# Optimization experiments

Hardware: AMD Instinct MI355X
Metric: run time of the kernel (lower is better)

## Reference

```python
import jax, jax.numpy as jnp
from jax import lax
import numpy as np

MAX_D = 4  # max_displacement


def conv3x3(x, w, b):
    # x: [B,Cin,H,W], w: [Cout,Cin,3,3], SAME padding (pad=1)
    y = lax.conv_general_dilated(
        x, w, window_strides=(1, 1), padding='SAME',
        dimension_numbers=('NCHW', 'OIHW', 'NCHW'))
    return y + b[None, :, None, None]


def compute_cost_volume(f1, f2, d):
    # roll+mask in the torch code == shift with zero padding:
    # cv[idx,h,w] = mean_c f1[c,h,w] * f2[c,h-i,w-j] (zero outside bounds)
    B, C, H, W = f1.shape
    pad = jnp.pad(f2, ((0, 0), (0, 0), (d, d), (d, d)))
    slices = []
    for i in range(-d, d + 1):
        for j in range(-d, d + 1):
            shifted = lax.dynamic_slice(pad, (0, 0, d - i, d - j), (B, C, H, W))
            slices.append((f1 * shifted).sum(axis=1) / C)  # [B,H,W]
    return jnp.stack(slices, axis=1)  # [B,81,H,W]


def setup_inputs() -> dict:
    key = jax.random.key(0)
    ks = jax.random.split(key, 10)
    B, C, H, W = 16, 64, 128, 128
    cv_ch = (2 * MAX_D + 1) ** 2  # 81
    def w_init(k, shape):
        fan_in = shape[1] * shape[2] * shape[3]
        return jax.random.normal(k, shape, dtype=jnp.float32) * np.float32(np.sqrt(2.0 / fan_in))
    return {
        'f1': jax.random.normal(ks[0], (B, C, H, W), dtype=jnp.float32),
        'f2_warped': jax.random.normal(ks[1], (B, C, H, W), dtype=jnp.float32),
        'w1': w_init(ks[2], (128, C + cv_ch, 3, 3)),
        'b1': jnp.zeros((128,), dtype=jnp.float32),
        'w2': w_init(ks[3], (64, 128, 3, 3)),
        'b2': jnp.zeros((64,), dtype=jnp.float32),
        'w3': w_init(ks[4], (32, 64, 3, 3)),
        'b3': jnp.zeros((32,), dtype=jnp.float32),
        'w4': w_init(ks[5], (2, 32, 3, 3)),
        'b4': jnp.zeros((2,), dtype=jnp.float32),
    }


def reference(f1, f2_warped, w1, b1, w2, b2, w3, b3, w4, b4):
    cv = compute_cost_volume(f1, f2_warped, MAX_D)       # [B,81,H,W]
    x = jnp.concatenate([f1, cv], axis=1)                # [B,145,H,W]
    x = jax.nn.relu(conv3x3(x, w1, b1))
    x = jax.nn.relu(conv3x3(x, w2, b2))
    x = jax.nn.relu(conv3x3(x, w3, b3))
    flow = conv3x3(x, w4, b4)                            # [B,2,H,W]
    return flow
```

## Files before the change

### kernel.cpp

```cpp
#include <hip/hip_runtime.h>


typedef __bf16 bf16x8 __attribute__((ext_vector_type(8)));
typedef float f32x4 __attribute__((ext_vector_type(4)));

__device__ __forceinline__ unsigned short f2bf_bits(float f) {
  unsigned int u = __float_as_uint(f);
  unsigned int r = (u + 0x7FFFu + ((u >> 16) & 1u)) >> 16;
  return (unsigned short)r;
}

__device__ __forceinline__ void glds16(const ushort* gp, ushort* lp) {
  __builtin_amdgcn_global_load_lds((const __attribute__((address_space(1))) void*)gp,
                                   (__attribute__((address_space(3))) void*)lp, 16, 0, 0);
}

__global__ void prep_w_kernel(const float* __restrict__ w, uint4* __restrict__ wp,
                              int CIN, int COUT, int CHUNKS, int NFRAG) {
  int idx = blockIdx.x * 256 + threadIdx.x;
  int total = CHUNKS * 9 * NFRAG * 64;
  if (idx >= total) return;
  int lane = idx & 63;
  int fi = idx >> 6;
  int nf = fi % NFRAG;
  int t = fi / NFRAG;
  int rs = t % 9;
  int c = t / 9;
  int co = nf * 16 + (lane & 15);
  int cib = c * 32 + (lane >> 4) * 8;
  union { uint4 q; ushort s[8]; } pk;
#pragma unroll
  for (int e = 0; e < 8; ++e) {
    int ci = cib + e;
    float v = (ci < CIN && co < COUT) ? w[(co * CIN + ci) * 9 + rs] : 0.f;
    pk.s[e] = f2bf_bits(v);
  }
  wp[idx] = pk.q;
}

__global__ __launch_bounds__(256) void pack_f1_kernel(const float* __restrict__ f1,
                                                      ushort* __restrict__ xf1) {
  __shared__ float tile[64][132];
  const int bid = blockIdx.x;
  const int h = bid & 127, b = bid >> 7;
  const int tid = threadIdx.x;
  for (int e = tid; e < 64 * 128; e += 256) {
    int c = e >> 7, w = e & 127;
    tile[c][w] = f1[((b * 64 + c) * 128 + h) * 128 + w];
  }
  __syncthreads();
  const int px = tid >> 1, cgb = (tid & 1) * 4;
  const long base = ((long)(b * 128 + h) * 128 + px) * 64;
#pragma unroll
  for (int e = 0; e < 4; ++e) {
    int c0 = (cgb + e) * 8;
    union { uint4 q; ushort s[8]; } pk;
#pragma unroll
    for (int k = 0; k < 8; ++k) pk.s[k] = f2bf_bits(tile[c0 + k][px]);
    *reinterpret_cast<uint4*>(&xf1[base + c0]) = pk.q;
  }
}

__global__ __launch_bounds__(256)
void cost_volume_kernel(const float* __restrict__ f1,
                        const float* __restrict__ f2,
                        ushort* __restrict__ xcv) {
  const int bx = blockIdx.x;
  const int idx = bx >> 3;
  const int b = 2 * (bx & 7) + (idx >> 6);
  const int h0 = (idx & 63) * 2;
  const int tid = threadIdx.x;
  const int q = tid & 31;
  const int rho = (tid >> 5) & 1;
  const int g = tid >> 6;

  __shared__ float arena[12480];

  float accF[2][9][4];
  float accP[3][4];
#pragma unroll
  for (int s = 0; s < 2; ++s)
#pragma unroll
    for (int jj = 0; jj < 9; ++jj)
#pragma unroll
      for (int e = 0; e < 4; ++e) accF[s][jj][e] = 0.f;
#pragma unroll
  for (int t = 0; t < 3; ++t)
#pragma unroll
    for (int e = 0; e < 4; ++e) accP[t][e] = 0.f;

  float st[13];

  auto stage = [&](int c) {
    const int cc = c * 2;
#pragma unroll
    for (int i = 0; i < 13; ++i) {
      int e = tid + i * 256;
      float v = 0.f;
      if (e < 2720) {
        int ci = e / 1360;
        int rem = e - ci * 1360;
        int a = rem / 136;
        int k = rem - a * 136;
        int gh = h0 - 4 + a, gw = k - 4;
        if ((unsigned)gh < 128u && (unsigned)gw < 128u)
          v = f2[((b * 64 + cc + ci) * 128 + gh) * 128 + gw];
      } else if (e < 3232) {
        int e2 = e - 2720;
        int ci = e2 >> 8, rr = (e2 >> 7) & 1, ww = e2 & 127;
        v = f1[((b * 64 + cc + ci) * 128 + h0 + rr) * 128 + ww];
      }
      st[i] = v;
    }
  };
  auto commit = [&](int bi) {
    float* bufp = arena + bi * 3232;
#pragma unroll
    for (int i = 0; i < 13; ++i) {
      int e = tid + i * 256;
      if (e < 3232) bufp[e] = st[i];
    }
  };

  stage(0);
  commit(0);

  for (int c = 0; c < 32; ++c) {
    __syncthreads();
    if (c < 31) stage(c + 1);
    const float* bufc = arena + (c & 1) * 3232;
#pragma unroll
    for (int ci = 0; ci < 2; ++ci) {
      const float* bp = bufc + ci * 1360;
      float4 f1q = *reinterpret_cast<const float4*>(bufc + 2720 + ci * 256 + rho * 128 + 4 * q);
      const float* f1e = &f1q.x;
#pragma unroll
      for (int s = 0; s < 2; ++s) {
        int a = rho + 8 - (2 * g + s);
        const float* rp = bp + a * 136 + 4 * q;
        float4 A = *reinterpret_cast<const float4*>(rp);
        float4 Bv = *reinterpret_cast<const float4*>(rp + 4);
        float4 Cv = *reinterpret_cast<const float4*>(rp + 8);
        float ev[12] = {A.x, A.y, A.z, A.w, Bv.x, Bv.y, Bv.z, Bv.w, Cv.x, Cv.y, Cv.z, Cv.w};
#pragma unroll
        for (int jj = 0; jj < 9; ++jj)
#pragma unroll
          for (int e = 0; e < 4; ++e)
            accF[s][jj][e] += f1e[e] * ev[8 - jj + e];
      }
      {
        const float* rp = bp + rho * 136 + 4 * q;
        if (g < 2) {
          float4 A = *reinterpret_cast<const float4*>(rp + 4);
          float4 Bv = *reinterpret_cast<const float4*>(rp + 8);
          float pv[8] = {A.x, A.y, A.z, A.w, Bv.x, Bv.y, Bv.z, Bv.w};
          if (g == 0) {
#pragma unroll
            for (int e = 0; e < 4; ++e) {
              accP[0][e] += f1e[e] * pv[4 + e];
              accP[1][e] += f1e[e] * pv[3 + e];
              accP[2][e] += f1e[e] * pv[2 + e];
            }
          } else {
#pragma unroll
            for (int e = 0; e < 4; ++e) {
              accP[0][e] += f1e[e] * pv[1 + e];
              accP[1][e] += f1e[e] * pv[e];
            }
          }
        } else {
          float4 A = *reinterpret_cast<const float4*>(rp);
          float4 Bv = *reinterpret_cast<const float4*>(rp + 4);
          float pv[8] = {A.x, A.y, A.z, A.w, Bv.x, Bv.y, Bv.z, Bv.w};
          if (g == 2) {
#pragma unroll
            for (int e = 0; e < 4; ++e) {
              accP[0][e] += f1e[e] * pv[3 + e];
              accP[1][e] += f1e[e] * pv[2 + e];
            }
          } else {
#pragma unroll
            for (int e = 0; e < 4; ++e) {
              accP[0][e] += f1e[e] * pv[1 + e];
              accP[1][e] += f1e[e] * pv[e];
            }
          }
        }
      }
    }
    if (c < 31) commit((c + 1) & 1);
  }

  __syncthreads();
  ushort* sO = (ushort*)arena;
  const float inv = 1.0f / 64.0f;
#pragma unroll
  for (int s = 0; s < 2; ++s) {
    int ch = (2 * g + s) * 9;
#pragma unroll
    for (int jj = 0; jj < 9; ++jj) {
      uint lo = (uint)f2bf_bits(accF[s][jj][0] * inv) | ((uint)f2bf_bits(accF[s][jj][1] * inv) << 16);
      uint hi = (uint)f2bf_bits(accF[s][jj][2] * inv) | ((uint)f2bf_bits(accF[s][jj][3] * inv) << 16);
      ushort* d = &sO[(rho * 96 + ch + jj) * 130 + 4 * q];
      *reinterpret_cast<uint*>(d) = lo;
      *reinterpret_cast<uint*>(d + 2) = hi;
    }
  }
  {
    const int npart = (g == 0) ? 3 : 2;
    const int chbase = 72 + ((g == 0) ? 0 : (g == 1) ? 3 : (g == 2) ? 5 : 7);
#pragma unroll
    for (int t = 0; t < 3; ++t) {
      if (t < npart) {
        uint lo = (uint)f2bf_bits(accP[t][0] * inv) | ((uint)f2bf_bits(accP[t][1] * inv) << 16);
        uint hi = (uint)f2bf_bits(accP[t][2] * inv) | ((uint)f2bf_bits(accP[t][3] * inv) << 16);
        ushort* d = &sO[(rho * 96 + chbase + t) * 130 + 4 * q];
        *reinterpret_cast<uint*>(d) = lo;
        *reinterpret_cast<uint*>(d + 2) = hi;
      }
    }
  }
  for (int e = tid; e < 1920; e += 256) {
    int r = e / 960;
    int rem = e - r * 960;
    int ch = 81 + (rem >> 6);
    int pxh = rem & 63;
    *reinterpret_cast<uint*>(&sO[(r * 96 + ch) * 130 + pxh * 2]) = 0u;
  }
  __syncthreads();

  {
    const int r = tid >> 7, u = tid & 127;
    uint4* dst = reinterpret_cast<uint4*>(xcv + ((long)(b * 128 + h0 + r) * 128) * 96);
#pragma unroll
    for (int j = 0; j < 12; ++j) {
      int t8 = 128 * j + u;
      int px = t8 / 12;
      int ch0 = (t8 - px * 12) * 8;
      union { uint4 qq; ushort ss[8]; } pk;
#pragma unroll
      for (int k = 0; k < 8; ++k) pk.ss[k] = sO[(r * 96 + ch0 + k) * 130 + px];
      dst[t8] = pk.qq;
    }
  }
}

template <int CA, int CB, int COUT, bool RELU, bool PLANAR>
__global__ __launch_bounds__(512, 2)
void conv_mfma_kernel(const ushort* __restrict__ xa, const ushort* __restrict__ xb,
                      const uint4* __restrict__ wp, const float* __restrict__ bias,
                      void* __restrict__ outv) {
  constexpr int CHUNKS = (CA + CB) / 32;
  constexpr int NFRAG = COUT / 16;
  constexpr int SXN = 4 * 130 * 32;
  constexpr int WTQ = 9 * NFRAG * 64;
  constexpr int WI = (WTQ + 511) / 512;
  constexpr int SO_STRIDE = COUT + 4;
  constexpr int STAGE_B = PLANAR ? 2048 : 2 * 128 * SO_STRIDE * 2;
  constexpr int SX_B = 2 * SXN * 2;
  constexpr int BASE_B = SX_B + WTQ * 16;
  constexpr int ARENA_B = STAGE_B > BASE_B ? STAGE_B : BASE_B;

  __shared__ __align__(16) char arena[ARENA_B];
  ushort* sXa = (ushort*)arena;
  ushort* sWt = (ushort*)(arena + SX_B);

  const int bx = blockIdx.x;
  const int idx = bx >> 3;
  const int b = 2 * (bx & 7) + (idx >> 6);
  const int h0 = (idx & 63) * 2;
  const int tid = threadIdx.x;
  const int lane = tid & 63;
  const int wid = tid >> 6;
  const int row = wid >> 2;
  const int m0 = (wid & 3) * 32;
  const int l15 = lane & 15;
  const int lg = lane >> 4;

  f32x4 acc[2][NFRAG];
#pragma unroll
  for (int mf = 0; mf < 2; ++mf)
#pragma unroll
    for (int nf = 0; nf < NFRAG; ++nf) acc[mf][nf] = {0.f, 0.f, 0.f, 0.f};

  if (tid < 64) {
    int bi = tid >> 5, tr = (tid >> 3) & 3, wz = (tid >> 2) & 1, gq = tid & 3;
    int wl = wz ? 129 : 0;
    *reinterpret_cast<uint4*>(&sXa[bi * SXN + ((tr * 130 + wl) * 4 + gq) * 8]) =
        make_uint4(0u, 0u, 0u, 0u);
  }
  if (h0 == 0 || h0 == 126) {
    const int trz = (h0 == 0) ? 0 : 3;
#pragma unroll
    for (int e = 0; e < 2; ++e) {
      int u = tid + e * 512;
      int bi = u >> 9, k = u & 511;
      *reinterpret_cast<uint4*>(&sXa[bi * SXN + ((trz * 130 + 1) * 4 + k) * 8]) =
          make_uint4(0u, 0u, 0u, 0u);
    }
  }

  auto stage = [&](int c, int bi) {
    const int c0 = c * 32;
    const ushort* src;
    int cst, coff;
    if (CB == 0 || c0 < CA) { src = xa; cst = CA; coff = c0; }
    else                    { src = xb; cst = CB; coff = c0 - CA; }
    const int tr = wid >> 1;
    const int gh = h0 - 1 + tr;
    if ((unsigned)gh < 128u) {
      const ushort* rowp = src + ((long)(b * 128 + gh) * 128) * cst + coff;
#pragma unroll
      for (int t = 0; t < 4; ++t) {
        int s = (wid & 1) * 4 + t;
        int u = s * 64 + lane;
        int wl = 1 + (u >> 2);
        int gq = lane & 3;
        int sw = (wl + (wl >> 2)) & 3;
        const ushort* gp = rowp + (long)(wl - 1) * cst + (gq ^ sw) * 8;
        ushort* lp = &sXa[bi * SXN + ((tr * 130 + 1) * 4 + s * 64) * 8];
        glds16(gp, lp);
      }
    }
  };

  auto stage_wt = [&](int c) {
    const ushort* src = (const ushort*)(wp + (size_t)c * WTQ);
#pragma unroll
    for (int i = 0; i < WI; ++i) {
      int e = tid + i * 512;
      if ((WTQ & 511) == 0 || e < WTQ)
        glds16(src + e * 8, sWt + (size_t)(tid & ~63) * 8 + (size_t)(i * 512) * 8);
    }
  };

  stage(0, 0);
  stage_wt(0);
  __syncthreads();

  for (int c = 0; c < CHUNKS; ++c) {
    if (c + 1 < CHUNKS) stage(c + 1, (c + 1) & 1);
    const int bi = c & 1;
#pragma unroll
    for (int rs = 0; rs < 9; ++rs) {
      const int r = rs / 3, s = rs % 3;
      const int tr = row + r;
      bf16x8 afr[2];
#pragma unroll
      for (int mf = 0; mf < 2; ++mf) {
        int wl = m0 + mf * 16 + l15 + s;
        int sw = (wl + (wl >> 2)) & 3;
        afr[mf] = *reinterpret_cast<const bf16x8*>(
            &sXa[bi * SXN + ((tr * 130 + wl) * 4 + (lg ^ sw)) * 8]);
      }
      const ushort* wrow = sWt + (size_t)(rs * NFRAG) * 64 * 8;
#pragma unroll
      for (int nf = 0; nf < NFRAG; ++nf) {
        bf16x8 bfr = *reinterpret_cast<const bf16x8*>(wrow + (nf * 64 + lane) * 8);
        acc[0][nf] = __builtin_amdgcn_mfma_f32_16x16x32_bf16(afr[0], bfr, acc[0][nf], 0, 0, 0);
        acc[1][nf] = __builtin_amdgcn_mfma_f32_16x16x32_bf16(afr[1], bfr, acc[1][nf], 0, 0, 0);
      }
    }
    __syncthreads();
    if (c + 1 < CHUNKS) stage_wt(c + 1);
    __syncthreads();
  }

  if (!PLANAR) {
    ushort* sO = (ushort*)arena;
#pragma unroll
    for (int nf = 0; nf < NFRAG; ++nf) {
      float bs = bias[nf * 16 + l15];
#pragma unroll
      for (int mf = 0; mf < 2; ++mf) {
        int px2 = row * 128 + m0 + mf * 16 + lg * 4;
#pragma unroll
        for (int j = 0; j < 4; ++j) {
          float v = acc[mf][nf][j] + bs;
          if (RELU) v = fmaxf(v, 0.f);
          sO[(px2 + j) * SO_STRIDE + nf * 16 + l15] = f2bf_bits(v);
        }
      }
    }
    __syncthreads();
    constexpr int QPP = COUT / 8;
    uint4* dst = reinterpret_cast<uint4*>((ushort*)outv + ((long)(b * 128 + h0) * 128) * COUT);
#pragma unroll
    for (int t0 = 0; t0 < 2 * 128 * QPP / 512; ++t0) {
      int t = t0 * 512 + tid;
      int px2 = t / QPP;
      int ch0 = (t & (QPP - 1)) * 8;
      union { uint4 qq; ushort ss[8]; } pk;
#pragma unroll
      for (int k = 0; k < 8; ++k) pk.ss[k] = sO[px2 * SO_STRIDE + ch0 + k];
      dst[t] = pk.qq;
    }
  } else {
    float* sF = (float*)arena;
    if (l15 < 2) {
#pragma unroll
      for (int mf = 0; mf < 2; ++mf) {
        int pxb = m0 + mf * 16 + lg * 4;
#pragma unroll
        for (int j = 0; j < 4; ++j)
          sF[(l15 * 2 + row) * 128 + pxb + j] = acc[mf][0][j] + bias[l15];
      }
    }
    __syncthreads();
    float* out = (float*)outv;
    if (tid < 128) {
      int ch = tid >> 6, r = (tid >> 5) & 1, qx = tid & 31;
      *reinterpret_cast<float4*>(&out[((long)(b * 2 + ch) * 128 + h0 + r) * 128 + qx * 4]) =
          *reinterpret_cast<float4*>(&sF[(ch * 2 + r) * 128 + qx * 4]);
    }
  }
}

extern "C" void kernel_launch(void* const* d_in, const int* in_sizes, int n_in,
                              void* d_out, int out_size, void* d_ws, size_t ws_size,
                              hipStream_t stream) {
  (void)in_sizes; (void)n_in; (void)out_size; (void)ws_size;
  const float* f1 = (const float*)d_in[0];
  const float* f2 = (const float*)d_in[1];
  const float* w1 = (const float*)d_in[2];
  const float* b1 = (const float*)d_in[3];
  const float* w2 = (const float*)d_in[4];
  const float* b2 = (const float*)d_in[5];
  const float* w3 = (const float*)d_in[6];
  const float* b3 = (const float*)d_in[7];
  const float* w4 = (const float*)d_in[8];
  const float* b4 = (const float*)d_in[9];

  char* ws = (char*)d_ws;
  size_t off = 0;
  ushort* xf1 = (ushort*)(ws + off); off += (size_t)262144 * 64 * 2;
  ushort* xcv = (ushort*)(ws + off); off += (size_t)262144 * 96 * 2;
  ushort* x1  = (ushort*)(ws + off); off += (size_t)262144 * 128 * 2;
  ushort* x2  = (ushort*)(ws + off); off += (size_t)262144 * 64 * 2;
  uint4* wp1 = (uint4*)(ws + off); off += (size_t)5 * 9 * 8 * 64 * 16;
  uint4* wp2 = (uint4*)(ws + off); off += (size_t)4 * 9 * 4 * 64 * 16;
  uint4* wp3 = (uint4*)(ws + off); off += (size_t)2 * 9 * 2 * 64 * 16;
  uint4* wp4 = (uint4*)(ws + off); off += (size_t)1 * 9 * 1 * 64 * 16;
  ushort* x3 = xf1;

  prep_w_kernel<<<90, 256, 0, stream>>>(w1, wp1, 145, 128, 5, 8);
  prep_w_kernel<<<36, 256, 0, stream>>>(w2, wp2, 128, 64, 4, 4);
  prep_w_kernel<<<9, 256, 0, stream>>>(w3, wp3, 64, 32, 2, 2);
  prep_w_kernel<<<3, 256, 0, stream>>>(w4, wp4, 32, 2, 1, 1);

  pack_f1_kernel<<<2048, 256, 0, stream>>>(f1, xf1);
  cost_volume_kernel<<<1024, 256, 0, stream>>>(f1, f2, xcv);

  conv_mfma_kernel<64, 96, 128, true, false><<<1024, 512, 0, stream>>>(xf1, xcv, wp1, b1, x1);
  conv_mfma_kernel<128, 0, 64, true, false><<<1024, 512, 0, stream>>>(x1, x1, wp2, b2, x2);
  conv_mfma_kernel<64, 0, 32, true, false><<<1024, 512, 0, stream>>>(x2, x2, wp3, b3, x3);
  conv_mfma_kernel<32, 0, 16, false, true><<<1024, 512, 0, stream>>>(x3, x3, wp4, b4, d_out);
}
```

Baseline: 332.2 us.

## Rebalance conv MFMA warp tiling and shrink cost-volume LDS staging

```diff
diff --git a/kernel.cpp b/kernel.cpp
--- a/kernel.cpp
+++ b/kernel.cpp
@@ -74,7 +74,7 @@
   const int rho = (tid >> 5) & 1;
   const int g = tid >> 6;
 
-  __shared__ float arena[12480];
+  __shared__ float arena[6464];
 
   float accF[2][9][4];
   float accP[3][4];
@@ -191,55 +191,54 @@
     if (c < 31) commit((c + 1) & 1);
   }
 
-  __syncthreads();
   ushort* sO = (ushort*)arena;
   const float inv = 1.0f / 64.0f;
 #pragma unroll
-  for (int s = 0; s < 2; ++s) {
-    int ch = (2 * g + s) * 9;
-#pragma unroll
-    for (int jj = 0; jj < 9; ++jj) {
-      uint lo = (uint)f2bf_bits(accF[s][jj][0] * inv) | ((uint)f2bf_bits(accF[s][jj][1] * inv) << 16);
-      uint hi = (uint)f2bf_bits(accF[s][jj][2] * inv) | ((uint)f2bf_bits(accF[s][jj][3] * inv) << 16);
-      ushort* d = &sO[(rho * 96 + ch + jj) * 130 + 4 * q];
-      *reinterpret_cast<uint*>(d) = lo;
-      *reinterpret_cast<uint*>(d + 2) = hi;
-    }
-  }
-  {
-    const int npart = (g == 0) ? 3 : 2;
-    const int chbase = 72 + ((g == 0) ? 0 : (g == 1) ? 3 : (g == 2) ? 5 : 7);
-#pragma unroll
-    for (int t = 0; t < 3; ++t) {
-      if (t < npart) {
-        uint lo = (uint)f2bf_bits(accP[t][0] * inv) | ((uint)f2bf_bits(accP[t][1] * inv) << 16);
-        uint hi = (uint)f2bf_bits(accP[t][2] * inv) | ((uint)f2bf_bits(accP[t][3] * inv) << 16);
-        ushort* d = &sO[(rho * 96 + chbase + t) * 130 + 4 * q];
-        *reinterpret_cast<uint*>(d) = lo;
-        *reinterpret_cast<uint*>(d + 2) = hi;
-      }
-    }
-  }
-  for (int e = tid; e < 1920; e += 256) {
-    int r = e / 960;
-    int rem = e - r * 960;
-    int ch = 81 + (rem >> 6);
-    int pxh = rem & 63;
-    *reinterpret_cast<uint*>(&sO[(r * 96 + ch) * 130 + pxh * 2]) = 0u;
-  }
-  __syncthreads();
-
-  {
-    const int r = tid >> 7, u = tid & 127;
+  for (int r = 0; r < 2; ++r) {
+    __syncthreads();
+    if (rho == r) {
+#pragma unroll
+      for (int s = 0; s < 2; ++s) {
+        int ch = (2 * g + s) * 9;
+#pragma unroll
+        for (int jj = 0; jj < 9; ++jj) {
+          uint lo = (uint)f2bf_bits(accF[s][jj][0] * inv) | ((uint)f2bf_bits(accF[s][jj][1] * inv) << 16);
+          uint hi = (uint)f2bf_bits(accF[s][jj][2] * inv) | ((uint)f2bf_bits(accF[s][jj][3] * inv) << 16);
+          ushort* d = &sO[(ch + jj) * 132 + 4 * q];
+          *reinterpret_cast<uint*>(d) = lo;
+          *reinterpret_cast<uint*>(d + 2) = hi;
+        }
+      }
+      const int npart = (g == 0) ? 3 : 2;
+      const int chbase = 72 + ((g == 0) ? 0 : (g == 1) ? 3 : (g == 2) ? 5 : 7);
+#pragma unroll
+      for (int t = 0; t < 3; ++t) {
+        if (t < npart) {
+          uint lo = (uint)f2bf_bits(accP[t][0] * inv) | ((uint)f2bf_bits(accP[t][1] * inv) << 16);
+          uint hi = (uint)f2bf_bits(accP[t][2] * inv) | ((uint)f2bf_bits(accP[t][3] * inv) << 16);
+          ushort* d = &sO[(chbase + t) * 132 + 4 * q];
+          *reinterpret_cast<uint*>(d) = lo;
+          *reinterpret_cast<uint*>(d + 2) = hi;
+        }
+      }
+    }
+    if (r == 0) {
+      for (int e = tid; e < 960; e += 256) {
+        int ch = 81 + (e >> 6);
+        int pxh = e & 63;
+        *reinterpret_cast<uint*>(&sO[ch * 132 + pxh * 2]) = 0u;
+      }
+    }
+    __syncthreads();
     uint4* dst = reinterpret_cast<uint4*>(xcv + ((long)(b * 128 + h0 + r) * 128) * 96);
 #pragma unroll
-    for (int j = 0; j < 12; ++j) {
-      int t8 = 128 * j + u;
+    for (int j = 0; j < 6; ++j) {
+      int t8 = 256 * j + tid;
       int px = t8 / 12;
       int ch0 = (t8 - px * 12) * 8;
       union { uint4 qq; ushort ss[8]; } pk;
 #pragma unroll
-      for (int k = 0; k < 8; ++k) pk.ss[k] = sO[(r * 96 + ch0 + k) * 130 + px];
+      for (int k = 0; k < 8; ++k) pk.ss[k] = sO[(ch0 + k) * 132 + px];
       dst[t8] = pk.qq;
     }
   }
@@ -252,6 +251,8 @@
                       void* __restrict__ outv) {
   constexpr int CHUNKS = (CA + CB) / 32;
   constexpr int NFRAG = COUT / 16;
+  constexpr int NFW = (NFRAG >= 2) ? NFRAG / 2 : 1;
+  constexpr int MFW = (NFRAG >= 2) ? 4 : 2;
   constexpr int SXN = 4 * 130 * 32;
   constexpr int WTQ = 9 * NFRAG * 64;
   constexpr int WI = (WTQ + 511) / 512;
@@ -272,16 +273,17 @@
   const int tid = threadIdx.x;
   const int lane = tid & 63;
   const int wid = tid >> 6;
-  const int row = wid >> 2;
-  const int m0 = (wid & 3) * 32;
   const int l15 = lane & 15;
   const int lg = lane >> 4;
-
-  f32x4 acc[2][NFRAG];
-#pragma unroll
-  for (int mf = 0; mf < 2; ++mf)
-#pragma unroll
-    for (int nf = 0; nf < NFRAG; ++nf) acc[mf][nf] = {0.f, 0.f, 0.f, 0.f};
+  const int cg    = (NFRAG >= 2) ? (wid >> 2) : 0;
+  const int row   = (NFRAG >= 2) ? ((wid >> 1) & 1) : (wid >> 2);
+  const int pbase = (NFRAG >= 2) ? ((wid & 1) * 64) : ((wid & 3) * 32);
+
+  f32x4 acc[MFW][NFW];
+#pragma unroll
+  for (int mf = 0; mf < MFW; ++mf)
+#pragma unroll
+    for (int nf = 0; nf < NFW; ++nf) acc[mf][nf] = {0.f, 0.f, 0.f, 0.f};
 
   if (tid < 64) {
     int bi = tid >> 5, tr = (tid >> 3) & 3, wz = (tid >> 2) & 1, gq = tid & 3;
@@ -345,20 +347,21 @@
     for (int rs = 0; rs < 9; ++rs) {
       const int r = rs / 3, s = rs % 3;
       const int tr = row + r;
-      bf16x8 afr[2];
-#pragma unroll
-      for (int mf = 0; mf < 2; ++mf) {
-        int wl = m0 + mf * 16 + l15 + s;
+      bf16x8 afr[MFW];
+#pragma unroll
+      for (int mf = 0; mf < MFW; ++mf) {
+        int wl = pbase + mf * 16 + l15 + s;
         int sw = (wl + (wl >> 2)) & 3;
         afr[mf] = *reinterpret_cast<const bf16x8*>(
             &sXa[bi * SXN + ((tr * 130 + wl) * 4 + (lg ^ sw)) * 8]);
       }
-      const ushort* wrow = sWt + (size_t)(rs * NFRAG) * 64 * 8;
-#pragma unroll
-      for (int nf = 0; nf < NFRAG; ++nf) {
+      const ushort* wrow = sWt + (size_t)(rs * NFRAG + cg * NFW) * 64 * 8;
+#pragma unroll
+      for (int nf = 0; nf < NFW; ++nf) {
         bf16x8 bfr = *reinterpret_cast<const bf16x8*>(wrow + (nf * 64 + lane) * 8);
-        acc[0][nf] = __builtin_amdgcn_mfma_f32_16x16x32_bf16(afr[0], bfr, acc[0][nf], 0, 0, 0);
-        acc[1][nf] = __builtin_amdgcn_mfma_f32_16x16x32_bf16(afr[1], bfr, acc[1][nf], 0, 0, 0);
+#pragma unroll
+        for (int mf = 0; mf < MFW; ++mf)
+          acc[mf][nf] = __builtin_amdgcn_mfma_f32_16x16x32_bf16(afr[mf], bfr, acc[mf][nf], 0, 0, 0);
       }
     }
     __syncthreads();
@@ -369,16 +372,16 @@
   if (!PLANAR) {
     ushort* sO = (ushort*)arena;
 #pragma unroll
-    for (int nf = 0; nf < NFRAG; ++nf) {
-      float bs = bias[nf * 16 + l15];
-#pragma unroll
-      for (int mf = 0; mf < 2; ++mf) {
-        int px2 = row * 128 + m0 + mf * 16 + lg * 4;
+    for (int nf = 0; nf < NFW; ++nf) {
+      float bs = bias[cg * NFW * 16 + nf * 16 + l15];
+#pragma unroll
+      for (int mf = 0; mf < MFW; ++mf) {
+        int px2 = row * 128 + pbase + mf * 16 + lg * 4;
 #pragma unroll
         for (int j = 0; j < 4; ++j) {
           float v = acc[mf][nf][j] + bs;
           if (RELU) v = fmaxf(v, 0.f);
-          sO[(px2 + j) * SO_STRIDE + nf * 16 + l15] = f2bf_bits(v);
+          sO[(px2 + j) * SO_STRIDE + cg * NFW * 16 + nf * 16 + l15] = f2bf_bits(v);
         }
       }
     }
@@ -399,8 +402,8 @@
     float* sF = (float*)arena;
     if (l15 < 2) {
 #pragma unroll
-      for (int mf = 0; mf < 2; ++mf) {
-        int pxb = m0 + mf * 16 + lg * 4;
+      for (int mf = 0; mf < MFW; ++mf) {
+        int pxb = pbase + mf * 16 + lg * 4;
 #pragma unroll
         for (int j = 0; j < 4; ++j)
           sF[(l15 * 2 + row) * 128 + pxb + j] = acc[mf][0][j] + bias[l15];
```

Measured after the change: 335.4 us. No clear change (+1.0%).
